# Kernel tuning notes

Measured on AMD Instinct MI355X. Metric: run time of the kernel, lower is better.

The kernel has to match this reference:

```python
import jax, jax.numpy as jnp
import numpy as np

Q = 128      # number of slices
S = 8        # slice_length = C // Q = 1024 // 128
H = 32       # unit_dim[0]
BN_EPS = 1e-3  # Keras BatchNormalization default epsilon


def setup_inputs() -> dict:
    key = jax.random.key(0)
    ks = jax.random.split(key, 5)
    B = 32768
    x = jax.random.normal(ks[0], (B, 1, 1, Q * S), dtype=jnp.float32)
    # Per-slice (grouped) parameters for the q=128 independent MLPs.
    W1 = jax.random.normal(ks[1], (Q, S, H), dtype=jnp.float32) / np.sqrt(S)
    b1 = jnp.zeros((Q, H), dtype=jnp.float32)
    gamma = jnp.ones((Q, H), dtype=jnp.float32)
    beta = jnp.zeros((Q, H), dtype=jnp.float32)
    mov_mean = 0.1 * jax.random.normal(ks[2], (Q, H), dtype=jnp.float32)
    mov_var = jnp.ones((Q, H), dtype=jnp.float32) + 0.1 * jax.random.uniform(ks[3], (Q, H), dtype=jnp.float32)
    W2 = jax.random.normal(ks[4], (Q, H, 1), dtype=jnp.float32) / np.sqrt(H)
    b2 = jnp.zeros((Q, 1), dtype=jnp.float32)
    return {"x": x, "W1": W1, "b1": b1, "gamma": gamma, "beta": beta,
            "mov_mean": mov_mean, "mov_var": mov_var, "W2": W2, "b2": b2}


def reference(x, W1, b1, gamma, beta, mov_mean, mov_var, W2, b2):
    B = x.shape[0]
    xs = x.reshape(B, Q, -1)                       # (B, Q, S)
    # Grouped Dense(32) + ELU, all 128 slices in one batched matmul
    h = jnp.einsum('bqs,qsh->bqh', xs, W1) + b1    # (B, Q, H)
    h = jax.nn.elu(h)
    # BatchNormalization (inference: moving statistics)
    inv = gamma * jax.lax.rsqrt(mov_var + BN_EPS)  # (Q, H)
    h = (h - mov_mean) * inv + beta
    # Grouped Dense(1)
    out = jnp.einsum('bqh,qho->bqo', h, W2) + b2   # (B, Q, 1)
    return out[..., 0]                              # (B, Q)
```

## Files before the change

kernel.cpp:

```cpp
#include <hip/hip_runtime.h>
#include <hip/hip_bf16.h>


#define QN 128
#define SN 8
#define HN 32
#define XROW 1024
#define BN_EPS 1e-3f

typedef short bf16x8 __attribute__((ext_vector_type(8)));
typedef float f32x16 __attribute__((ext_vector_type(16)));
typedef unsigned int u32;

#define WS_A_BYTES (QN * 64 * 16)
#define WS_C_OFF   WS_A_BYTES
#define WS_C_BYTES (QN * 32 * 4)
#define WS_W_OFF   (WS_C_OFF + WS_C_BYTES)
#define WS_W_BYTES (QN * 32 * 4)
#define WS_B2_OFF  (WS_W_OFF + WS_W_BYTES)

static __device__ __forceinline__ u32 pkbf(float lo, float hi) {
    union { __hip_bfloat162 h2; u32 u; } c;
    c.h2 = __float22bfloat162_rn(float2{lo, hi});
    return c.u;
}

__global__ void divenc_prep(const float* __restrict__ W1, const float* __restrict__ b1,
                            const float* __restrict__ gamma_, const float* __restrict__ beta_,
                            const float* __restrict__ mmean, const float* __restrict__ mvar,
                            const float* __restrict__ W2, const float* __restrict__ b2,
                            unsigned char* __restrict__ ws)
{
    const int q = blockIdx.x;
    const int m = threadIdx.x;

    u32 d0 = 0, d1 = 0, d2 = 0, d3 = 0;
    if (m < 32) {
        d0 = pkbf(W1[(q*SN + 0)*HN + m], W1[(q*SN + 1)*HN + m]);
        d1 = pkbf(W1[(q*SN + 2)*HN + m], W1[(q*SN + 3)*HN + m]);
        d2 = pkbf(W1[(q*SN + 4)*HN + m], W1[(q*SN + 5)*HN + m]);
        d3 = pkbf(W1[(q*SN + 6)*HN + m], W1[(q*SN + 7)*HN + m]);
    }
    ((uint4*)ws)[q*64 + m] = uint4{d0, d1, d2, d3};

    float* wsC  = (float*)(ws + WS_C_OFF);
    float* wsW  = (float*)(ws + WS_W_OFF);
    float* wsB2 = (float*)(ws + WS_B2_OFF);
    if (m < 32) {
        const int half = m >> 4, r = m & 15;
        const int h = (r & 3) + 8*(r >> 2) + 4*half;
        wsC[q*32 + m] = b1[q*HN + h];
        float inv = gamma_[q*HN+h] * rsqrtf(mvar[q*HN+h] + BN_EPS);
        wsW[q*32 + m] = inv * W2[q*HN + h];
    }
    if (m == 0) {
        float acc = b2[q];
        for (int h = 0; h < HN; ++h) {
            float inv = gamma_[q*HN+h] * rsqrtf(mvar[q*HN+h] + BN_EPS);
            acc += (beta_[q*HN+h] - mmean[q*HN+h]*inv) * W2[q*HN+h];
        }
        wsB2[q] = acc;
    }
}

__global__ __launch_bounds__(512, 4)
void divenc_mfma(const float* __restrict__ x, const unsigned char* __restrict__ ws,
                 float* __restrict__ out)
{
    const int lane = threadIdx.x & 63;
    const int wv   = threadIdx.x >> 6;
    const int half = lane >> 5;
    const int bl   = lane & 31;
    const int b0   = blockIdx.x * 256;
    const int q0   = blockIdx.y * 32;

    const uint4* wsA  = (const uint4*)ws;
    const float* wsC  = (const float*)(ws + WS_C_OFF);
    const float* wsW  = (const float*)(ws + WS_W_OFF);
    const float* wsB2 = (const float*)(ws + WS_B2_OFF);

    __shared__ float slab[2][256][9];

    #pragma unroll
    for (int qg = 0; qg < 4; ++qg) {
        const int q = q0 + qg*8 + wv;

        union { uint4 u; bf16x8 v; } A1, A2;
        A1.u = wsA[q*64 + lane];
        A2.u = wsA[q*64 + (lane ^ 32)];

        f32x16 cini;
        const float* cp_ = wsC + q*32 + half*16;
        #pragma unroll
        for (int r = 0; r < 16; ++r) cini[r] = cp_[r];
        float w2r[16];
        const float* wp_ = wsW + q*32 + half*16;
        #pragma unroll
        for (int r = 0; r < 16; ++r) w2r[r] = wp_[r];
        const float b2p = wsB2[q];

        const float* xq = x + (size_t)b0 * XROW + q * SN;
        float4 xa = *(const float4*)(xq + (size_t)lane * XROW);
        float4 xc = *(const float4*)(xq + (size_t)lane * XROW + 4);

        #pragma unroll
        for (int sub = 0; sub < 4; ++sub) {
            const int nsub = (sub < 3) ? sub + 1 : sub;
            const float* np = xq + (size_t)(nsub*64 + lane) * XROW;
            float4 na = *(const float4*)np;
            float4 nc = *(const float4*)(np + 4);

            union { uint4 u; bf16x8 v; } B;
            B.u = uint4{ pkbf(xa.x, xa.y), pkbf(xa.z, xa.w),
                         pkbf(xc.x, xc.y), pkbf(xc.z, xc.w) };

            f32x16 D0 = __builtin_amdgcn_mfma_f32_32x32x16_bf16(A1.v, B.v, cini, 0, 0, 0);
            f32x16 D1 = __builtin_amdgcn_mfma_f32_32x32x16_bf16(A2.v, B.v, cini, 0, 0, 0);

            float p0 = 0.f, p1 = 0.f;
            #pragma unroll
            for (int r = 0; r < 16; ++r) {
                float z0 = D0[r];
                float e0 = __expf(fminf(z0, 0.f)) - 1.f;
                p0 = fmaf(fmaxf(z0, e0), w2r[r], p0);
                float z1 = D1[r];
                float e1 = __expf(fminf(z1, 0.f)) - 1.f;
                p1 = fmaf(fmaxf(z1, e1), w2r[r], p1);
            }
            p0 += __shfl_xor(p0, 32);
            p1 += __shfl_xor(p1, 32);

            const float v = (half ? p1 : p0) + b2p;
            slab[qg & 1][sub*64 + half*32 + bl][wv] = v;

            xa = na; xc = nc;
        }

        __syncthreads();
        {
            const int row = threadIdx.x >> 1;
            const int cp  = (threadIdx.x & 1) * 4;
            float4 vv;
            vv.x = slab[qg & 1][row][cp + 0];
            vv.y = slab[qg & 1][row][cp + 1];
            vv.z = slab[qg & 1][row][cp + 2];
            vv.w = slab[qg & 1][row][cp + 3];
            *(float4*)(out + (size_t)(b0 + row) * QN + q0 + qg*8 + cp) = vv;
        }
    }
}

extern "C" void kernel_launch(void* const* d_in, const int* in_sizes, int n_in,
                              void* d_out, int out_size, void* d_ws, size_t ws_size,
                              hipStream_t stream) {
    const float* x      = (const float*)d_in[0];
    const float* W1     = (const float*)d_in[1];
    const float* b1     = (const float*)d_in[2];
    const float* gamma_ = (const float*)d_in[3];
    const float* beta_  = (const float*)d_in[4];
    const float* mmean  = (const float*)d_in[5];
    const float* mvar   = (const float*)d_in[6];
    const float* W2     = (const float*)d_in[7];
    const float* b2     = (const float*)d_in[8];
    float* out = (float*)d_out;
    unsigned char* ws = (unsigned char*)d_ws;

    const int Btot = in_sizes[0] / XROW;

    divenc_prep<<<QN, 64, 0, stream>>>(W1, b1, gamma_, beta_, mmean, mvar, W2, b2, ws);
    divenc_mfma<<<dim3(Btot / 256, QN / 32), 512, 0, stream>>>(x, ws, out);
}
```

Baseline: 49.91 us.

## Halve batch tile per block and restructure slice loop with single end sync

Each block now covers 128 batch rows instead of 256, which doubles the grid, and the launch bound is raised so more blocks can sit on each CU. The inner sub-loop becomes two explicit MFMA passes whose four x loads are issued together up front. The per-slice-group barrier and the double-buffered slab are replaced by one 128x32 slab that is written out with a single sync at the end. The second bias is split as half into each partial sum. The aim is more memory parallelism and fewer barriers, but the rolled qg loop gives up cross-iteration prefetch and weights are reloaded more often overall.

New measurement: 57.86 us. +15.9%, slower.

```diff
diff --git a/kernel.cpp b/kernel.cpp
--- a/kernel.cpp
+++ b/kernel.cpp
@@ -63,7 +63,7 @@
     }
 }
 
-__global__ __launch_bounds__(512, 4)
+__global__ __launch_bounds__(512, 6)
 void divenc_mfma(const float* __restrict__ x, const unsigned char* __restrict__ ws,
                  float* __restrict__ out)
 {
@@ -71,53 +71,41 @@
     const int wv   = threadIdx.x >> 6;
     const int half = lane >> 5;
     const int bl   = lane & 31;
-    const int b0   = blockIdx.x * 256;
+    const int b0   = blockIdx.x * 128;
     const int q0   = blockIdx.y * 32;
 
-    const uint4* wsA  = (const uint4*)ws;
-    const float* wsC  = (const float*)(ws + WS_C_OFF);
-    const float* wsW  = (const float*)(ws + WS_W_OFF);
-    const float* wsB2 = (const float*)(ws + WS_B2_OFF);
+    __shared__ float slab[128][36];
 
-    __shared__ float slab[2][256][9];
+    const uint4* wsA  = (const uint4*)ws + (size_t)(q0 + wv) * 64;
+    const float* wsC  = (const float*)(ws + WS_C_OFF) + (q0 + wv) * 32 + half * 16;
+    const float* wsW  = (const float*)(ws + WS_W_OFF) + (q0 + wv) * 32 + half * 16;
+    const float* wsB2 = (const float*)(ws + WS_B2_OFF) + (q0 + wv);
+    const float* xq   = x + (size_t)(b0 + lane) * XROW + (q0 + wv) * SN;
 
-    #pragma unroll
+    #pragma unroll 1
     for (int qg = 0; qg < 4; ++qg) {
-        const int q = q0 + qg*8 + wv;
+        float4 xa0 = *(const float4*)(xq);
+        float4 xc0 = *(const float4*)(xq + 4);
+        float4 xa1 = *(const float4*)(xq + 64 * XROW);
+        float4 xc1 = *(const float4*)(xq + 64 * XROW + 4);
 
         union { uint4 u; bf16x8 v; } A1, A2;
-        A1.u = wsA[q*64 + lane];
-        A2.u = wsA[q*64 + (lane ^ 32)];
+        A1.u = wsA[lane];
+        A2.u = wsA[lane ^ 32];
 
         f32x16 cini;
-        const float* cp_ = wsC + q*32 + half*16;
+        float w2r[16];
         #pragma unroll
-        for (int r = 0; r < 16; ++r) cini[r] = cp_[r];
-        float w2r[16];
-        const float* wp_ = wsW + q*32 + half*16;
-        #pragma unroll
-        for (int r = 0; r < 16; ++r) w2r[r] = wp_[r];
-        const float b2p = wsB2[q];
+        for (int r = 0; r < 16; ++r) { cini[r] = wsC[r]; w2r[r] = wsW[r]; }
+        const float hb2 = 0.5f * wsB2[0];
 
-        const float* xq = x + (size_t)b0 * XROW + q * SN;
-        float4 xa = *(const float4*)(xq + (size_t)lane * XROW);
-        float4 xc = *(const float4*)(xq + (size_t)lane * XROW + 4);
-
-        #pragma unroll
-        for (int sub = 0; sub < 4; ++sub) {
-            const int nsub = (sub < 3) ? sub + 1 : sub;
-            const float* np = xq + (size_t)(nsub*64 + lane) * XROW;
-            float4 na = *(const float4*)np;
-            float4 nc = *(const float4*)(np + 4);
-
+        {
             union { uint4 u; bf16x8 v; } B;
-            B.u = uint4{ pkbf(xa.x, xa.y), pkbf(xa.z, xa.w),
-                         pkbf(xc.x, xc.y), pkbf(xc.z, xc.w) };
-
+            B.u = uint4{ pkbf(xa0.x, xa0.y), pkbf(xa0.z, xa0.w),
+                         pkbf(xc0.x, xc0.y), pkbf(xc0.z, xc0.w) };
             f32x16 D0 = __builtin_amdgcn_mfma_f32_32x32x16_bf16(A1.v, B.v, cini, 0, 0, 0);
             f32x16 D1 = __builtin_amdgcn_mfma_f32_32x32x16_bf16(A2.v, B.v, cini, 0, 0, 0);
-
-            float p0 = 0.f, p1 = 0.f;
+            float p0 = hb2, p1 = hb2;
             #pragma unroll
             for (int r = 0; r < 16; ++r) {
                 float z0 = D0[r];
@@ -129,24 +117,49 @@
             }
             p0 += __shfl_xor(p0, 32);
             p1 += __shfl_xor(p1, 32);
-
-            const float v = (half ? p1 : p0) + b2p;
-            slab[qg & 1][sub*64 + half*32 + bl][wv] = v;
-
-            xa = na; xc = nc;
+            slab[half*32 + bl][qg*8 + wv] = half ? p1 : p0;
         }
 
-        __syncthreads();
         {
-            const int row = threadIdx.x >> 1;
-            const int cp  = (threadIdx.x & 1) * 4;
-            float4 vv;
-            vv.x = slab[qg & 1][row][cp + 0];
-            vv.y = slab[qg & 1][row][cp + 1];
-            vv.z = slab[qg & 1][row][cp + 2];
-            vv.w = slab[qg & 1][row][cp + 3];
-            *(float4*)(out + (size_t)(b0 + row) * QN + q0 + qg*8 + cp) = vv;
+            union { uint4 u; bf16x8 v; } B;
+            B.u = uint4{ pkbf(xa1.x, xa1.y), pkbf(xa1.z, xa1.w),
+                         pkbf(xc1.x, xc1.y), pkbf(xc1.z, xc1.w) };
+            f32x16 D0 = __builtin_amdgcn_mfma_f32_32x32x16_bf16(A1.v, B.v, cini, 0, 0, 0);
+            f32x16 D1 = __builtin_amdgcn_mfma_f32_32x32x16_bf16(A2.v, B.v, cini, 0, 0, 0);
+            float p0 = hb2, p1 = hb2;
+            #pragma unroll
+            for (int r = 0; r < 16; ++r) {
+                float z0 = D0[r];
+                float e0 = __expf(fminf(z0, 0.f)) - 1.f;
+                p0 = fmaf(fmaxf(z0, e0), w2r[r], p0);
+                float z1 = D1[r];
+                float e1 = __expf(fminf(z1, 0.f)) - 1.f;
+                p1 = fmaf(fmaxf(z1, e1), w2r[r], p1);
+            }
+            p0 += __shfl_xor(p0, 32);
+            p1 += __shfl_xor(p1, 32);
+            slab[64 + half*32 + bl][qg*8 + wv] = half ? p1 : p0;
         }
+
+        xq  += 64;
+        wsA += 8 * 64;
+        wsC += 8 * 32;
+        wsW += 8 * 32;
+        wsB2 += 8;
+    }
+
+    __syncthreads();
+
+    #pragma unroll
+    for (int p = 0; p < 2; ++p) {
+        const int row  = (threadIdx.x >> 3) + p * 64;
+        const int col4 = (threadIdx.x & 7) * 4;
+        float4 vv;
+        vv.x = slab[row][col4 + 0];
+        vv.y = slab[row][col4 + 1];
+        vv.z = slab[row][col4 + 2];
+        vv.w = slab[row][col4 + 3];
+        *(float4*)(out + (size_t)(b0 + row) * QN + q0 + col4) = vv;
     }
 }
 
@@ -168,5 +181,5 @@
     const int Btot = in_sizes[0] / XROW;
 
     divenc_prep<<<QN, 64, 0, stream>>>(W1, b1, gamma_, beta_, mmean, mvar, W2, b2, ws);
-    divenc_mfma<<<dim3(Btot / 256, QN / 32), 512, 0, stream>>>(x, ws, out);
+    divenc_mfma<<<dim3(Btot / 128, QN / 32), 512, 0, stream>>>(x, ws, out);
 }
```

## Prefetch x three steps ahead across slice groups and simplify ELU epilogue

Applied to the files above, without the earlier changes.

The x loads now run through a 4-slot register ring that stays three iterations ahead across all slice groups, not just one sub-tile ahead within a group. The qg loop is no longer unrolled. ELU is split as max(z,0)+exp(min(z,0)), and the constant -1 term is folded into the precomputed output bias. The two MFMAs and their epilogues are sequenced separately. The per-group barrier and store are replaced by one barrier and wider stores from a larger shared slab. This aims to hide global-load latency and cut barriers, at the cost of more registers and LDS, which may limit occupancy.

Measured after the change: 52.51 us. +5.2%, slower.

```diff
diff --git a/kernel.cpp b/kernel.cpp
--- a/kernel.cpp
+++ b/kernel.cpp
@@ -57,7 +57,8 @@
         float acc = b2[q];
         for (int h = 0; h < HN; ++h) {
             float inv = gamma_[q*HN+h] * rsqrtf(mvar[q*HN+h] + BN_EPS);
-            acc += (beta_[q*HN+h] - mmean[q*HN+h]*inv) * W2[q*HN+h];
+            float w2p = inv * W2[q*HN + h];
+            acc += (beta_[q*HN+h] - mmean[q*HN+h]*inv) * W2[q*HN+h] - w2p;
         }
         wsB2[q] = acc;
     }
@@ -67,8 +68,9 @@
 void divenc_mfma(const float* __restrict__ x, const unsigned char* __restrict__ ws,
                  float* __restrict__ out)
 {
-    const int lane = threadIdx.x & 63;
-    const int wv   = threadIdx.x >> 6;
+    const int tid  = threadIdx.x;
+    const int lane = tid & 63;
+    const int wv   = tid >> 6;
     const int half = lane >> 5;
     const int bl   = lane & 31;
     const int b0   = blockIdx.x * 256;
@@ -79,9 +81,19 @@
     const float* wsW  = (const float*)(ws + WS_W_OFF);
     const float* wsB2 = (const float*)(ws + WS_B2_OFF);
 
-    __shared__ float slab[2][256][9];
+    __shared__ float slab[4][256][9];
 
+    const float* xbase = x + (size_t)(b0 + lane) * XROW + (q0 + wv) * SN;
+
+    float4 sa[4], sc[4];
     #pragma unroll
+    for (int p = 0; p < 3; ++p) {
+        const float* a = xbase + (size_t)(p * 64) * XROW;
+        sa[p] = *(const float4*)a;
+        sc[p] = *(const float4*)(a + 4);
+    }
+
+    #pragma unroll 1
     for (int qg = 0; qg < 4; ++qg) {
         const int q = q0 + qg*8 + wv;
 
@@ -99,53 +111,67 @@
         for (int r = 0; r < 16; ++r) w2r[r] = wp_[r];
         const float b2p = wsB2[q];
 
-        const float* xq = x + (size_t)b0 * XROW + q * SN;
-        float4 xa = *(const float4*)(xq + (size_t)lane * XROW);
-        float4 xc = *(const float4*)(xq + (size_t)lane * XROW + 4);
-
         #pragma unroll
         for (int sub = 0; sub < 4; ++sub) {
-            const int nsub = (sub < 3) ? sub + 1 : sub;
-            const float* np = xq + (size_t)(nsub*64 + lane) * XROW;
-            float4 na = *(const float4*)np;
-            float4 nc = *(const float4*)(np + 4);
+            {
+                const int it = qg*4 + sub;
+                const int n  = (it + 3 < 16) ? it + 3 : 15;
+                const int slot = (sub + 3) & 3;
+                const float* a = xbase + (size_t)((n & 3) * 64) * XROW + (n >> 2) * 64;
+                sa[slot] = *(const float4*)a;
+                sc[slot] = *(const float4*)(a + 4);
+            }
 
             union { uint4 u; bf16x8 v; } B;
-            B.u = uint4{ pkbf(xa.x, xa.y), pkbf(xa.z, xa.w),
-                         pkbf(xc.x, xc.y), pkbf(xc.z, xc.w) };
+            B.u = uint4{ pkbf(sa[sub].x, sa[sub].y), pkbf(sa[sub].z, sa[sub].w),
+                         pkbf(sc[sub].x, sc[sub].y), pkbf(sc[sub].z, sc[sub].w) };
 
             f32x16 D0 = __builtin_amdgcn_mfma_f32_32x32x16_bf16(A1.v, B.v, cini, 0, 0, 0);
-            f32x16 D1 = __builtin_amdgcn_mfma_f32_32x32x16_bf16(A2.v, B.v, cini, 0, 0, 0);
-
-            float p0 = 0.f, p1 = 0.f;
+            float p0 = 0.f, p0b = 0.f;
             #pragma unroll
             for (int r = 0; r < 16; ++r) {
-                float z0 = D0[r];
-                float e0 = __expf(fminf(z0, 0.f)) - 1.f;
-                p0 = fmaf(fmaxf(z0, e0), w2r[r], p0);
-                float z1 = D1[r];
-                float e1 = __expf(fminf(z1, 0.f)) - 1.f;
-                p1 = fmaf(fmaxf(z1, e1), w2r[r], p1);
+                const float z = D0[r];
+                const float E = __expf(fminf(z, 0.f));
+                const float R = fmaxf(z, 0.f);
+                p0  = fmaf(E, w2r[r], p0);
+                p0b = fmaf(R, w2r[r], p0b);
             }
+            p0 += p0b;
             p0 += __shfl_xor(p0, 32);
+
+            f32x16 D1 = __builtin_amdgcn_mfma_f32_32x32x16_bf16(A2.v, B.v, cini, 0, 0, 0);
+            float p1 = 0.f, p1b = 0.f;
+            #pragma unroll
+            for (int r = 0; r < 16; ++r) {
+                const float z = D1[r];
+                const float E = __expf(fminf(z, 0.f));
+                const float R = fmaxf(z, 0.f);
+                p1  = fmaf(E, w2r[r], p1);
+                p1b = fmaf(R, w2r[r], p1b);
+            }
+            p1 += p1b;
             p1 += __shfl_xor(p1, 32);
 
             const float v = (half ? p1 : p0) + b2p;
-            slab[qg & 1][sub*64 + half*32 + bl][wv] = v;
+            slab[qg][sub*64 + half*32 + bl][wv] = v;
+        }
+    }
 
-            xa = na; xc = nc;
-        }
+    __syncthreads();
 
-        __syncthreads();
-        {
-            const int row = threadIdx.x >> 1;
-            const int cp  = (threadIdx.x & 1) * 4;
+    {
+        const int row = tid >> 1;
+        const int h16 = (tid & 1) * 16;
+        float* orow = out + (size_t)(b0 + row) * QN + q0 + h16;
+        #pragma unroll
+        for (int c4 = 0; c4 < 4; ++c4) {
+            const int c = h16 + c4 * 4;
             float4 vv;
-            vv.x = slab[qg & 1][row][cp + 0];
-            vv.y = slab[qg & 1][row][cp + 1];
-            vv.z = slab[qg & 1][row][cp + 2];
-            vv.w = slab[qg & 1][row][cp + 3];
-            *(float4*)(out + (size_t)(b0 + row) * QN + q0 + qg*8 + cp) = vv;
+            vv.x = slab[c >> 3][row][(c & 7) + 0];
+            vv.y = slab[c >> 3][row][(c & 7) + 1];
+            vv.z = slab[c >> 3][row][(c & 7) + 2];
+            vv.w = slab[c >> 3][row][(c & 7) + 3];
+            *(float4*)(orow + c4 * 4) = vv;
         }
     }
 }
```
